# Kernel optimization log

Measured on AMD Instinct MI355X. Metric: run time of the kernel, lower is better.

Reference implementation:

```python
import math
import jax, jax.numpy as jnp
import numpy as np

D_MODEL = 1024
N_HEADS = 16
HEAD_DIM = D_MODEL // N_HEADS  # 64
QDIM = HEAD_DIM // 4           # 16
SPIKE_SLOPE = 5.0
B, S = 2, 2048


def _qweight(r, i, j, k):
    # Hamilton-product weight matrix, identical to QLinear.forward's torch.cat construction.
    return jnp.concatenate([
        jnp.concatenate([r, -i, -j, -k], 1),
        jnp.concatenate([i, r, -k, j], 1),
        jnp.concatenate([j, k, r, -i], 1),
        jnp.concatenate([k, -j, i, r], 1),
    ], 0)


def setup_inputs() -> dict:
    key = jax.random.key(0)
    ks = jax.random.split(key, 20)
    Qo = Qi = D_MODEL // 4  # 256
    p = lambda k, shape, s=0.02: (jax.random.normal(k, shape, dtype=jnp.float32) * s)
    inp = {
        'query': jax.random.normal(ks[0], (B, S, D_MODEL), dtype=jnp.float32),
        'key_in': jax.random.normal(ks[1], (B, S, D_MODEL), dtype=jnp.float32),
        'value': jax.random.normal(ks[2], (B, S, D_MODEL), dtype=jnp.float32),
        'mask': jnp.ones((B, S), dtype=jnp.int32),
        'density_feat': jax.random.normal(ks[3], (B, S, 3), dtype=jnp.float32),
        # q_proj QLinear params
        'wq_r': p(ks[4], (Qo, Qi)), 'wq_i': p(ks[5], (Qo, Qi)),
        'wq_j': p(ks[6], (Qo, Qi)), 'wq_k': p(ks[7], (Qo, Qi)),
        'bq': jnp.zeros((D_MODEL,), jnp.float32),
        # k_proj QLinear params
        'wk_r': p(ks[8], (Qo, Qi)), 'wk_i': p(ks[9], (Qo, Qi)),
        'wk_j': p(ks[10], (Qo, Qi)), 'wk_k': p(ks[11], (Qo, Qi)),
        'bk': jnp.zeros((D_MODEL,), jnp.float32),
        # v_proj / out_proj dense params
        'wv': p(ks[12], (D_MODEL, D_MODEL)), 'bv': jnp.zeros((D_MODEL,), jnp.float32),
        'wo': p(ks[13], (D_MODEL, D_MODEL)), 'bo': jnp.zeros((D_MODEL,), jnp.float32),
        # learned spike threshold (init -1.0 as in torch)
        'threshold': jnp.asarray(-1.0, dtype=jnp.float32),
        # density_mod MLP (use nonzero values so the gate shift is exercised)
        'dm1_w': p(ks[14], (16, 3), 0.5), 'dm1_b': p(ks[15], (16,), 0.1),
        'dm2_w': p(ks[16], (1, 16), 0.5), 'dm2_b': p(ks[17], (1,), 0.1),
    }
    return inp


def reference(query, key_in, value, mask, density_feat,
              wq_r, wq_i, wq_j, wq_k, bq,
              wk_r, wk_i, wk_j, wk_k, bk,
              wv, bv, wo, bo, threshold,
              dm1_w, dm1_b, dm2_w, dm2_b):
    H, hd, Qd = N_HEADS, HEAD_DIM, QDIM
    Bq, Sq, D = query.shape

    Wq = _qweight(wq_r, wq_i, wq_j, wq_k)
    Wk = _qweight(wk_r, wk_i, wk_j, wk_k)
    q = query @ Wq.T + bq
    k = key_in @ Wk.T + bk
    v = value @ wv.T + bv

    # head-major split, matching torch.cat(x.split(hd, -1), dim=0)
    qh = q.reshape(Bq, Sq, H, hd).transpose(2, 0, 1, 3)  # (H,B,S,hd)
    kh = k.reshape(Bq, Sq, H, hd).transpose(2, 0, 1, 3)
    vh = v.reshape(Bq, Sq, H, hd).transpose(2, 0, 1, 3)

    # sum of 4 quaternion-component dot products == full dot product over hd
    scores = jnp.einsum('hbmd,hbnd->hbmn', qh, kh) / math.sqrt(Qd)
    scores = jnp.clip(scores, -6.0, 6.0)

    base_threshold = jax.nn.softplus(threshold)
    h1 = jax.nn.gelu(density_feat @ dm1_w.T + dm1_b, approximate=False)
    d_shift = (h1 @ dm2_w.T + dm2_b)[..., 0]  # (B,N)
    thr = base_threshold + d_shift[None, :, None, :] * 0.1  # (1,B,1,N)

    spike_gate = jax.nn.sigmoid(SPIKE_SLOPE * (scores - thr))
    mod = scores * (1.0 + spike_gate * 2.0)

    m2 = (mask[:, :, None] * mask[:, None, :])[None]  # (1,B,N,N)
    mod = jnp.where(m2 == 0, -10000.0, mod)

    weights = jax.nn.softmax(jnp.clip(mod, -30.0, 30.0), axis=-1)
    # dropout: eval mode (identity)
    out_h = jnp.einsum('hbmn,hbnd->hbmd', weights, vh)
    out = out_h.transpose(1, 2, 0, 3).reshape(Bq, Sq, D)
    return out @ wo.T + bo
```

## Files before the change

### kernel.cpp

```cpp
#include <hip/hip_runtime.h>
#include <stdint.h>
#include <math.h>

#define BB 2
#define SS 2048
#define DM 1024
#define NH 16
#define HD 64
#define MTOT (BB*SS)

typedef __bf16 bf16x8 __attribute__((ext_vector_type(8)));
typedef float  f32x4  __attribute__((ext_vector_type(4)));
typedef uint32_t u32x4 __attribute__((ext_vector_type(4)));

__device__ __forceinline__ unsigned short f2bf(float f) {
  __bf16 h = (__bf16)f;
  return __builtin_bit_cast(unsigned short, h);
}

__device__ __forceinline__ bf16x8 ldsv8(const unsigned short* p) {
  return __builtin_bit_cast(bf16x8, *(const u32x4*)p);
}

__device__ __forceinline__ void gl16(const void* g, void* l) {
  __builtin_amdgcn_global_load_lds(
      (const __attribute__((address_space(1))) uint32_t*)g,
      (__attribute__((address_space(3))) uint32_t*)l, 16, 0, 0);
}

#define MFMA16(a,b,c) __builtin_amdgcn_mfma_f32_16x16x32_bf16((a),(b),(c),0,0,0)

#define C_NEG5L2E  (-7.213475204444817f)
#define C_L2E      (1.4426950408889634f)
#define C_18L2E    (25.968510736001341f)

__global__ __launch_bounds__(256) void cvt_bf16(
    const float* __restrict__ a, const float* __restrict__ b, const float* __restrict__ c,
    unsigned short* __restrict__ ao, unsigned short* __restrict__ bo, unsigned short* __restrict__ co)
{
  const int i8 = (blockIdx.x * 256 + threadIdx.x) * 8;
  {
    const float4 f0 = *(const float4*)(a + i8);
    const float4 f1 = *(const float4*)(a + i8 + 4);
    union { unsigned short us[8]; u32x4 v; } t;
    t.us[0]=f2bf(f0.x); t.us[1]=f2bf(f0.y); t.us[2]=f2bf(f0.z); t.us[3]=f2bf(f0.w);
    t.us[4]=f2bf(f1.x); t.us[5]=f2bf(f1.y); t.us[6]=f2bf(f1.z); t.us[7]=f2bf(f1.w);
    *(u32x4*)(ao + i8) = t.v;
  }
  {
    const float4 f0 = *(const float4*)(b + i8);
    const float4 f1 = *(const float4*)(b + i8 + 4);
    union { unsigned short us[8]; u32x4 v; } t;
    t.us[0]=f2bf(f0.x); t.us[1]=f2bf(f0.y); t.us[2]=f2bf(f0.z); t.us[3]=f2bf(f0.w);
    t.us[4]=f2bf(f1.x); t.us[5]=f2bf(f1.y); t.us[6]=f2bf(f1.z); t.us[7]=f2bf(f1.w);
    *(u32x4*)(bo + i8) = t.v;
  }
  {
    const float4 f0 = *(const float4*)(c + i8);
    const float4 f1 = *(const float4*)(c + i8 + 4);
    union { unsigned short us[8]; u32x4 v; } t;
    t.us[0]=f2bf(f0.x); t.us[1]=f2bf(f0.y); t.us[2]=f2bf(f0.z); t.us[3]=f2bf(f0.w);
    t.us[4]=f2bf(f1.x); t.us[5]=f2bf(f1.y); t.us[6]=f2bf(f1.z); t.us[7]=f2bf(f1.w);
    *(u32x4*)(co + i8) = t.v;
  }
}

__global__ __launch_bounds__(256) void prep_w(
    const float* __restrict__ wqr, const float* __restrict__ wqi,
    const float* __restrict__ wqj, const float* __restrict__ wqk,
    const float* __restrict__ wkr, const float* __restrict__ wki,
    const float* __restrict__ wkj, const float* __restrict__ wkk,
    const float* __restrict__ wv,  const float* __restrict__ wo,
    unsigned short* __restrict__ Wq, unsigned short* __restrict__ Wk,
    unsigned short* __restrict__ Wv, unsigned short* __restrict__ Wo)
{
  const int idx = blockIdx.x * 256 + threadIdx.x;
  const int o = idx >> 10, i = idx & 1023;
  const int br = o >> 8, bc = i >> 8;
  const int ro = o & 255, ci = i & 255;
  const int comp[4][4] = {{0,1,2,3},{1,0,3,2},{2,3,0,1},{3,2,1,0}};
  const float sgn[4][4] = {{1.f,-1.f,-1.f,-1.f},{1.f,1.f,-1.f,1.f},{1.f,1.f,1.f,-1.f},{1.f,-1.f,1.f,1.f}};
  const float* pq[4] = {wqr, wqi, wqj, wqk};
  const float* pk[4] = {wkr, wki, wkj, wkk};
  const int c_ = comp[br][bc];
  const float s_ = sgn[br][bc];
  const int pidx = ro * 256 + ci;
  Wq[idx] = f2bf(s_ * pq[c_][pidx]);
  Wk[idx] = f2bf(s_ * pk[c_][pidx]);
  Wv[idx] = f2bf(wv[idx]);
  Wo[idx] = f2bf(wo[idx]);
}

__global__ __launch_bounds__(256) void prep_thr(
    const float* __restrict__ density, const float* __restrict__ dm1w,
    const float* __restrict__ dm1b, const float* __restrict__ dm2w,
    const float* __restrict__ dm2b, const float* __restrict__ thr_s,
    const int* __restrict__ mask, float2* __restrict__ out)
{
  const int i = blockIdx.x * 256 + threadIdx.x;
  if (i >= BB * SS) return;
  const float x0 = density[i*3+0], x1 = density[i*3+1], x2 = density[i*3+2];
  const float base = log1pf(expf(thr_s[0]));
  float acc = dm2b[0];
  #pragma unroll
  for (int j = 0; j < 16; ++j) {
    const float hj = dm1w[j*3+0]*x0 + dm1w[j*3+1]*x1 + dm1w[j*3+2]*x2 + dm1b[j];
    const float ge = 0.5f * hj * (1.0f + erff(hj * 0.70710678118654752f));
    acc += dm2w[j] * ge;
  }
  const float thr = base + 0.1f * acc;
  out[i] = make_float2(thr * (-C_NEG5L2E),
                       mask[i] ? 1e30f : -30.0f);
}

struct GemmArgs {
  const unsigned short* A[3];
  const unsigned short* W[3];
  const float* bias[3];
  void* out[3];
  float scale[3];
  int omode[3];
};

template<int DB>
__global__ __launch_bounds__(256) void gemm_bt(GemmArgs args)
{
  __shared__ __align__(16) unsigned short lA[DB + 1][128*64];
  __shared__ __align__(16) unsigned short lB[DB + 1][128*64];
  const int z = blockIdx.y;
  const int tid = threadIdx.x;
  const int wid = tid >> 6, lane = tid & 63;
  const int l15 = lane & 15, l4 = lane >> 4;
  const int bm = blockIdx.x & 31, bn = blockIdx.x >> 5;
  const int row0 = bm * 128, col0 = bn * 128;
  const int wm = (wid >> 1) * 64, wn = (wid & 1) * 64;

  const unsigned short* gA[4];
  const unsigned short* gB[4];
  #pragma unroll
  for (int i = 0; i < 4; ++i) {
    const int c = (wid * 4 + i) * 64 + lane;
    const int r = c >> 3, jx = c & 7, j = jx ^ (r & 7);
    gA[i] = args.A[z] + (row0 + r) * 1024 + j * 8;
    gB[i] = args.W[z] + (col0 + r) * 1024 + j * 8;
  }

  f32x4 acc[4][4];
  #pragma unroll
  for (int i = 0; i < 4; ++i)
    #pragma unroll
    for (int j = 0; j < 4; ++j) acc[i][j] = (f32x4){0.f,0.f,0.f,0.f};

  #pragma unroll
  for (int i = 0; i < 4; ++i) {
    gl16(gA[i], &lA[0][(wid * 4 + i) * 512]);
    gl16(gB[i], &lB[0][(wid * 4 + i) * 512]);
  }
  if (DB) __syncthreads();

  for (int kt = 0; kt < 16; ++kt) {
    const int cb = DB ? (kt & 1) : 0;
    if (DB) {
      if (kt < 15) {
        const int nb = cb ^ 1, k0 = (kt + 1) * 64;
        #pragma unroll
        for (int i = 0; i < 4; ++i) {
          gl16(gA[i] + k0, &lA[nb][(wid * 4 + i) * 512]);
          gl16(gB[i] + k0, &lB[nb][(wid * 4 + i) * 512]);
        }
      }
    } else {
      if (kt > 0) {
        const int k0 = kt * 64;
        #pragma unroll
        for (int i = 0; i < 4; ++i) {
          gl16(gA[i] + k0, &lA[0][(wid * 4 + i) * 512]);
          gl16(gB[i] + k0, &lB[0][(wid * 4 + i) * 512]);
        }
      }
      __syncthreads();
    }
    #pragma unroll
    for (int kk = 0; kk < 2; ++kk) {
      const int kl = kk * 32 + l4 * 8;
      bf16x8 af[4], bfb[4];
      #pragma unroll
      for (int mi = 0; mi < 4; ++mi) {
        const int r = wm + mi * 16 + l15;
        af[mi] = ldsv8(&lA[cb][r * 64 + (kl ^ ((r & 7) << 3))]);
      }
      #pragma unroll
      for (int nj = 0; nj < 4; ++nj) {
        const int r = wn + nj * 16 + l15;
        bfb[nj] = ldsv8(&lB[cb][r * 64 + (kl ^ ((r & 7) << 3))]);
      }
      #pragma unroll
      for (int mi = 0; mi < 4; ++mi)
        #pragma unroll
        for (int nj = 0; nj < 4; ++nj)
          acc[mi][nj] = MFMA16(af[mi], bfb[nj], acc[mi][nj]);
    }
    __syncthreads();
  }

  const int om = args.omode[z];
  const float sc = args.scale[z];
  void* Cptr = args.out[z];
  #pragma unroll
  for (int nj = 0; nj < 4; ++nj) {
    const int c = col0 + wn + nj * 16 + l15;
    const float bv_ = args.bias[z][c];
    #pragma unroll
    for (int mi = 0; mi < 4; ++mi) {
      const int rb = row0 + wm + mi * 16 + l4 * 4;
      #pragma unroll
      for (int e = 0; e < 4; ++e) {
        const float val = (acc[mi][nj][e] + bv_) * sc;
        const int r = rb + e;
        if (om == 0) {
          ((unsigned short*)Cptr)[r * 1024 + c] = f2bf(val);
        } else if (om == 2) {
          ((float*)Cptr)[r * 1024 + c] = val;
        } else {
          const int h = c >> 6, d = c & 63, b = r >> 11, s = r & 2047;
          ((unsigned short*)Cptr)[((h * BB + b) * HD + d) * SS + s] = f2bf(val);
        }
      }
    }
  }
}

__global__ __launch_bounds__(512) void attn_kernel(
    const unsigned short* __restrict__ qg, const unsigned short* __restrict__ kg,
    const unsigned short* __restrict__ vT, const float2* __restrict__ klim,
    const int* __restrict__ mask, unsigned short* __restrict__ outg)
{
  __shared__ __align__(16) unsigned short smem[20480];
  unsigned short* lK = smem;
  unsigned short* lV = smem + 8192;
  unsigned short* lP = smem + 16384;

  const int tid = threadIdx.x;
  const int wid = tid >> 6, lane = tid & 63;
  const int l15 = lane & 15, l4 = lane >> 4;
  const int rg = wid >> 1, par = wid & 1;
  const int hb = blockIdx.x & 31, qb = blockIdx.x >> 5;
  const int h = hb >> 1, b = hb & 1;
  const int qr0 = qb * 64 + rg * 16;

  const int kcr = tid >> 3, kcj = (tid & 7) * 8;
  const int vcd = tid >> 3, vck = (tid & 7) * 8;
  const int kdst = (kcr >> 5) * 2048 + (kcr & 31) * 64 + (kcj ^ ((((kcr & 31) >> 1) & 7) << 3));
  const int vdst = (vck >> 5) * 2048 + vcd * 32 + ((vck & 31) ^ ((vcd & 3) << 3));

  const unsigned short* kbase = kg + (b * SS) * DM + h * HD;
  const unsigned short* vbase = vT + ((h * BB + b) * HD) * SS;
  const float2* klimb = klim + b * SS;

  bf16x8 aq[2];
  {
    const unsigned short* qs = qg + (b * SS + qr0 + l15) * DM + h * HD + l4 * 8;
    aq[0] = __builtin_bit_cast(bf16x8, *(const u32x4*)qs);
    aq[1] = __builtin_bit_cast(bf16x8, *(const u32x4*)(qs + 32));
  }
  float limq[4];
  #pragma unroll
  for (int e = 0; e < 4; ++e)
    limq[e] = mask[b * SS + qr0 + l4 * 4 + e] ? 1e30f : -30.0f;

  float lrun[4] = {0.f, 0.f, 0.f, 0.f};
  f32x4 o[4];
  #pragma unroll
  for (int d = 0; d < 4; ++d) o[d] = (f32x4){0.f,0.f,0.f,0.f};

  unsigned short* lPw = lP + wid * 512;

  u32x4 kr = *(const u32x4*)(kbase + kcr * DM + kcj);
  u32x4 vr = *(const u32x4*)(vbase + vcd * SS + vck);
  *(u32x4*)&lK[kdst] = kr;
  *(u32x4*)&lV[vdst] = vr;
  __syncthreads();

  for (int pr = 0; pr < 32; ++pr) {
    const int cur = pr & 1;
    const unsigned short* lKt = lK + cur * 4096 + par * 2048;
    const unsigned short* lVt = lV + cur * 4096 + par * 2048;
    const int n0 = pr * 64 + par * 32;

    if (pr < 31) {
      const int nn = (pr + 1) * 64;
      kr = *(const u32x4*)(kbase + (nn + kcr) * DM + kcj);
      vr = *(const u32x4*)(vbase + vcd * SS + nn + vck);
    }

    const float4 klA = *(const float4*)(klimb + n0 + 2 * l15);

    f32x4 sv[2];
    __builtin_amdgcn_s_setprio(1);
    #pragma unroll
    for (int cf = 0; cf < 2; ++cf) {
      f32x4 a = (f32x4){0.f,0.f,0.f,0.f};
      const int r = 2 * l15 + cf;
      #pragma unroll
      for (int kk = 0; kk < 2; ++kk)
        a = MFMA16(aq[kk], ldsv8(&lKt[r * 64 + ((kk * 32 + l4 * 8) ^ ((l15 & 7) << 3))]), a);
      sv[cf] = a;
    }
    __builtin_amdgcn_s_setprio(0);

    float pvv[2][4];
    #pragma unroll
    for (int cf = 0; cf < 2; ++cf) {
      const float kth = cf ? klA.z : klA.x;
      const float klm = cf ? klA.w : klA.y;
      #pragma unroll
      for (int e = 0; e < 4; ++e) {
        float s = fminf(fmaxf(sv[cf][e], -6.f), 6.f);
        const float t = __builtin_amdgcn_exp2f(fmaf(s, C_NEG5L2E, kth));
        const float g = __builtin_amdgcn_rcpf(1.f + t);
        float md = fmaf(s + s, g, s);
        md = fminf(md, fminf(klm, limq[e]));
        const float p = __builtin_amdgcn_exp2f(fmaf(md, C_L2E, -C_18L2E));
        pvv[cf][e] = p;
        lrun[e] += p;
      }
    }

    #pragma unroll
    for (int e = 0; e < 4; ++e) {
      const int rr = l4 * 4 + e;
      union { unsigned short us[2]; unsigned int u; } pk2;
      pk2.us[0] = f2bf(pvv[0][e]);
      pk2.us[1] = f2bf(pvv[1][e]);
      *(unsigned int*)&lPw[rr * 32 + ((2 * l15) ^ ((rr & 3) << 3))] = pk2.u;
    }
    asm volatile("s_waitcnt lgkmcnt(0)" ::: "memory");
    __builtin_amdgcn_sched_barrier(0);

    const bf16x8 pa = ldsv8(&lPw[l15 * 32 + ((l4 * 8) ^ ((l15 & 3) << 3))]);

    __builtin_amdgcn_s_setprio(1);
    #pragma unroll
    for (int df = 0; df < 4; ++df) {
      const int d = df * 16 + l15;
      o[df] = MFMA16(pa, ldsv8(&lVt[d * 32 + ((l4 * 8) ^ ((d & 3) << 3))]), o[df]);
    }
    __builtin_amdgcn_s_setprio(0);

    if (pr < 31) {
      const int nxt = cur ^ 1;
      *(u32x4*)&lK[nxt * 4096 + kdst] = kr;
      *(u32x4*)&lV[nxt * 4096 + vdst] = vr;
    }
    __syncthreads();
  }

  __syncthreads();
  float* xch = (float*)smem;
  float* slot = xch + rg * 1280;
  if (par) {
    #pragma unroll
    for (int df = 0; df < 4; ++df)
      *(f32x4*)&slot[(df * 64 + lane) * 4] = o[df];
    f32x4 lr;
    lr[0] = lrun[0]; lr[1] = lrun[1]; lr[2] = lrun[2]; lr[3] = lrun[3];
    *(f32x4*)&slot[1024 + lane * 4] = lr;
  }
  __syncthreads();
  if (!par) {
    #pragma unroll
    for (int df = 0; df < 4; ++df) {
      const f32x4 t = *(const f32x4*)&slot[(df * 64 + lane) * 4];
      o[df][0] += t[0]; o[df][1] += t[1]; o[df][2] += t[2]; o[df][3] += t[3];
    }
    const f32x4 lr = *(const f32x4*)&slot[1024 + lane * 4];
    #pragma unroll
    for (int e = 0; e < 4; ++e) {
      float ls = lrun[e] + lr[e];
      ls += __shfl_xor(ls, 1);
      ls += __shfl_xor(ls, 2);
      ls += __shfl_xor(ls, 4);
      ls += __shfl_xor(ls, 8);
      const float rl = __builtin_amdgcn_rcpf(ls);
      const int r = qr0 + l4 * 4 + e;
      #pragma unroll
      for (int df = 0; df < 4; ++df) {
        outg[(b * SS + r) * DM + h * HD + df * 16 + l15] = f2bf(o[df][e] * rl);
      }
    }
  }
}

extern "C" void kernel_launch(void* const* d_in, const int* in_sizes, int n_in,
                              void* d_out, int out_size, void* d_ws, size_t ws_size,
                              hipStream_t stream)
{
  const float* query   = (const float*)d_in[0];
  const float* key_in  = (const float*)d_in[1];
  const float* value   = (const float*)d_in[2];
  const int*   mask    = (const int*)d_in[3];
  const float* density = (const float*)d_in[4];
  const float* wq_r = (const float*)d_in[5];
  const float* wq_i = (const float*)d_in[6];
  const float* wq_j = (const float*)d_in[7];
  const float* wq_k = (const float*)d_in[8];
  const float* bq   = (const float*)d_in[9];
  const float* wk_r = (const float*)d_in[10];
  const float* wk_i = (const float*)d_in[11];
  const float* wk_j = (const float*)d_in[12];
  const float* wk_k = (const float*)d_in[13];
  const float* bk   = (const float*)d_in[14];
  const float* wv   = (const float*)d_in[15];
  const float* bv   = (const float*)d_in[16];
  const float* wo   = (const float*)d_in[17];
  const float* bo   = (const float*)d_in[18];
  const float* thrs = (const float*)d_in[19];
  const float* dm1w = (const float*)d_in[20];
  const float* dm1b = (const float*)d_in[21];
  const float* dm2w = (const float*)d_in[22];
  const float* dm2b = (const float*)d_in[23];

  char* ws = (char*)d_ws;
  unsigned short* Wq  = (unsigned short*)(ws + ((size_t)0 << 20));
  unsigned short* Wk  = (unsigned short*)(ws + ((size_t)2 << 20));
  unsigned short* Wv  = (unsigned short*)(ws + ((size_t)4 << 20));
  unsigned short* Wo  = (unsigned short*)(ws + ((size_t)6 << 20));
  unsigned short* qbf = (unsigned short*)(ws + ((size_t)8 << 20));
  unsigned short* kbf = (unsigned short*)(ws + ((size_t)16 << 20));
  unsigned short* vT  = (unsigned short*)(ws + ((size_t)24 << 20));
  unsigned short* att = (unsigned short*)(ws + ((size_t)32 << 20));
  float2* klim        = (float2*)(ws + ((size_t)40 << 20));

  unsigned short* qcv = (unsigned short*)d_out;
  unsigned short* kcv = (unsigned short*)d_out + (size_t)MTOT * DM;
  unsigned short* vcv = att;

  cvt_bf16<<<2048, 256, 0, stream>>>(query, key_in, value, qcv, kcv, vcv);
  prep_w<<<4096, 256, 0, stream>>>(wq_r, wq_i, wq_j, wq_k,
                                   wk_r, wk_i, wk_j, wk_k,
                                   wv, wo, Wq, Wk, Wv, Wo);
  prep_thr<<<16, 256, 0, stream>>>(density, dm1w, dm1b, dm2w, dm2b, thrs, mask, klim);

  GemmArgs qkv;
  qkv.A[0] = qcv; qkv.W[0] = Wq; qkv.bias[0] = bq; qkv.out[0] = qbf; qkv.scale[0] = 0.25f; qkv.omode[0] = 0;
  qkv.A[1] = kcv; qkv.W[1] = Wk; qkv.bias[1] = bk; qkv.out[1] = kbf; qkv.scale[1] = 1.0f;  qkv.omode[1] = 0;
  qkv.A[2] = vcv; qkv.W[2] = Wv; qkv.bias[2] = bv; qkv.out[2] = vT;  qkv.scale[2] = 1.0f;  qkv.omode[2] = 1;
  gemm_bt<0><<<dim3(256, 3), 256, 0, stream>>>(qkv);

  attn_kernel<<<1024, 512, 0, stream>>>(qbf, kbf, vT, klim, mask, att);

  GemmArgs og;
  og.A[0] = att; og.W[0] = Wo; og.bias[0] = bo; og.out[0] = d_out; og.scale[0] = 1.0f; og.omode[0] = 2;
  og.A[1] = att; og.W[1] = Wo; og.bias[1] = bo; og.out[1] = d_out; og.scale[1] = 1.0f; og.omode[1] = 2;
  og.A[2] = att; og.W[2] = Wo; og.bias[2] = bo; og.out[2] = d_out; og.scale[2] = 1.0f; og.omode[2] = 2;
  gemm_bt<1><<<dim3(256, 1), 256, 0, stream>>>(og);
}
```

Measured before the change: 188.3 us.

## Rework attention to 32x32 MFMA with register P exchange and mask-free fast path

The attention kernel switches from 16x16x32 to 32x32x16 MFMA tiles, with each block covering 128 query rows. The P matrix is now passed between lanes with cross-lane shuffles instead of a round trip through LDS. Key thresholds and mask limits are staged in LDS alongside K/V. A per-64-key bitmap built in prep_thr lets tiles with no masked keys skip the key-mask min. The aim is fewer LDS round trips and instructions per tile, in exchange for half as many blocks and more register pressure.

After: 233.5 us. 24.0% more time.

```diff
diff --git a/kernel.cpp b/kernel.cpp
--- a/kernel.cpp
+++ b/kernel.cpp
@@ -11,6 +11,7 @@
 
 typedef __bf16 bf16x8 __attribute__((ext_vector_type(8)));
 typedef float  f32x4  __attribute__((ext_vector_type(4)));
+typedef float  f32x16 __attribute__((ext_vector_type(16)));
 typedef uint32_t u32x4 __attribute__((ext_vector_type(4)));
 
 __device__ __forceinline__ unsigned short f2bf(float f) {
@@ -29,6 +30,7 @@
 }
 
 #define MFMA16(a,b,c) __builtin_amdgcn_mfma_f32_16x16x32_bf16((a),(b),(c),0,0,0)
+#define MFMA32(a,b,c) __builtin_amdgcn_mfma_f32_32x32x16_bf16((a),(b),(c),0,0,0)
 
 #define C_NEG5L2E  (-7.213475204444817f)
 #define C_L2E      (1.4426950408889634f)
@@ -95,7 +97,8 @@
     const float* __restrict__ density, const float* __restrict__ dm1w,
     const float* __restrict__ dm1b, const float* __restrict__ dm2w,
     const float* __restrict__ dm2b, const float* __restrict__ thr_s,
-    const int* __restrict__ mask, float2* __restrict__ out)
+    const int* __restrict__ mask, float* __restrict__ kth,
+    float* __restrict__ klm, unsigned int* __restrict__ fbits)
 {
   const int i = blockIdx.x * 256 + threadIdx.x;
   if (i >= BB * SS) return;
@@ -109,8 +112,12 @@
     acc += dm2w[j] * ge;
   }
   const float thr = base + 0.1f * acc;
-  out[i] = make_float2(thr * (-C_NEG5L2E),
-                       mask[i] ? 1e30f : -30.0f);
+  const int mk = mask[i];
+  kth[i] = thr * (-C_NEG5L2E);
+  klm[i] = mk ? 1e30f : -30.0f;
+  const unsigned long long any = __ballot(mk == 0);
+  if ((threadIdx.x & 63) == 0 && any)
+    atomicOr(&fbits[i >> 11], 1u << ((i >> 6) & 31));
 }
 
 struct GemmArgs {
@@ -230,163 +237,199 @@
   }
 }
 
-__global__ __launch_bounds__(512) void attn_kernel(
+__global__ __launch_bounds__(512, 4) void attn_kernel(
     const unsigned short* __restrict__ qg, const unsigned short* __restrict__ kg,
-    const unsigned short* __restrict__ vT, const float2* __restrict__ klim,
-    const int* __restrict__ mask, unsigned short* __restrict__ outg)
+    const unsigned short* __restrict__ vT, const float* __restrict__ kth_g,
+    const float* __restrict__ klm_g, const unsigned int* __restrict__ fbits,
+    unsigned short* __restrict__ outg)
 {
-  __shared__ __align__(16) unsigned short smem[20480];
-  unsigned short* lK = smem;
-  unsigned short* lV = smem + 8192;
-  unsigned short* lP = smem + 16384;
-
+  __shared__ __align__(16) unsigned char smem[36864];
   const int tid = threadIdx.x;
-  const int wid = tid >> 6, lane = tid & 63;
-  const int l15 = lane & 15, l4 = lane >> 4;
+  const int lane = tid & 63, wid = tid >> 6;
+  const int l31 = lane & 31, l5 = lane >> 5;
   const int rg = wid >> 1, par = wid & 1;
-  const int hb = blockIdx.x & 31, qb = blockIdx.x >> 5;
+  const int hb = blockIdx.x & 31, qc = blockIdx.x >> 5;
   const int h = hb >> 1, b = hb & 1;
-  const int qr0 = qb * 64 + rg * 16;
-
-  const int kcr = tid >> 3, kcj = (tid & 7) * 8;
-  const int vcd = tid >> 3, vck = (tid & 7) * 8;
-  const int kdst = (kcr >> 5) * 2048 + (kcr & 31) * 64 + (kcj ^ ((((kcr & 31) >> 1) & 7) << 3));
-  const int vdst = (vck >> 5) * 2048 + vcd * 32 + ((vck & 31) ^ ((vcd & 3) << 3));
-
-  const unsigned short* kbase = kg + (b * SS) * DM + h * HD;
-  const unsigned short* vbase = vT + ((h * BB + b) * HD) * SS;
-  const float2* klimb = klim + b * SS;
-
-  bf16x8 aq[2];
+  const int qr0 = qc * 128 + rg * 32;
+
+  const unsigned short* kbase = kg + (size_t)(b * SS) * DM + h * HD;
+  const unsigned short* vbase = vT + (size_t)((h * BB + b) * HD) * SS;
+  const float* kthb = kth_g + b * SS;
+  const float* klmb = klm_g + b * SS;
+  const unsigned int fb = fbits[b];
+
+  const int sk = tid >> 3, sj = tid & 7;
+  const int kp = sk >> 5, kkl = sk & 31;
+  const int kdst = kp*4096 + (kkl>>1)*256 + (((((kkl&1)<<3)|sj)) ^ ((kkl>>1)&15))*16;
+  const int vp = sj >> 2, vjj = sj & 3;
+  const int vdst = 8192 + vp*4096 + (sk>>2)*256 + (((((sk&3)<<2)|vjj)) ^ ((sk>>2)&15))*16;
+  const unsigned short* kgsrc = kbase + sk * DM + sj * 8;
+  const unsigned short* vgsrc = vbase + (size_t)sk * SS + sj * 8;
+
+  bf16x8 bq[4];
   {
-    const unsigned short* qs = qg + (b * SS + qr0 + l15) * DM + h * HD + l4 * 8;
-    aq[0] = __builtin_bit_cast(bf16x8, *(const u32x4*)qs);
-    aq[1] = __builtin_bit_cast(bf16x8, *(const u32x4*)(qs + 32));
-  }
-  float limq[4];
-  #pragma unroll
-  for (int e = 0; e < 4; ++e)
-    limq[e] = mask[b * SS + qr0 + l4 * 4 + e] ? 1e30f : -30.0f;
-
-  float lrun[4] = {0.f, 0.f, 0.f, 0.f};
-  f32x4 o[4];
-  #pragma unroll
-  for (int d = 0; d < 4; ++d) o[d] = (f32x4){0.f,0.f,0.f,0.f};
-
-  unsigned short* lPw = lP + wid * 512;
-
-  u32x4 kr = *(const u32x4*)(kbase + kcr * DM + kcj);
-  u32x4 vr = *(const u32x4*)(vbase + vcd * SS + vck);
-  *(u32x4*)&lK[kdst] = kr;
-  *(u32x4*)&lV[vdst] = vr;
+    const unsigned short* qs = qg + (size_t)(b * SS + qr0 + l31) * DM + h * HD + l5 * 8;
+    #pragma unroll
+    for (int ks = 0; ks < 4; ++ks)
+      bq[ks] = __builtin_bit_cast(bf16x8, *(const u32x4*)(qs + ks * 16));
+  }
+  const float limq = klmb[qr0 + l31];
+
+  f32x16 O0 = {}, O1 = {};
+  float lsum = 0.f;
+
+  u32x4 kr = *(const u32x4*)kgsrc;
+  u32x4 vr = *(const u32x4*)vgsrc;
+  f32x4 tk, tl;
+  if (tid < 16)      tk = *(const f32x4*)(kthb + tid * 4);
+  else if (tid < 32) tl = *(const f32x4*)(klmb + (tid - 16) * 4);
+  *(u32x4*)(smem + kdst) = kr;
+  *(u32x4*)(smem + vdst) = vr;
+  if (tid < 16)      *(f32x4*)(smem + 16384 + tid * 16) = tk;
+  else if (tid < 32) *(f32x4*)(smem + 16640 + (tid - 16) * 16) = tl;
   __syncthreads();
 
   for (int pr = 0; pr < 32; ++pr) {
-    const int cur = pr & 1;
-    const unsigned short* lKt = lK + cur * 4096 + par * 2048;
-    const unsigned short* lVt = lV + cur * 4096 + par * 2048;
-    const int n0 = pr * 64 + par * 32;
+    unsigned char* cb = smem + (pr & 1) * 16896;
+    const int n0 = pr * 64;
 
     if (pr < 31) {
-      const int nn = (pr + 1) * 64;
-      kr = *(const u32x4*)(kbase + (nn + kcr) * DM + kcj);
-      vr = *(const u32x4*)(vbase + vcd * SS + nn + vck);
-    }
-
-    const float4 klA = *(const float4*)(klimb + n0 + 2 * l15);
-
-    f32x4 sv[2];
-    __builtin_amdgcn_s_setprio(1);
-    #pragma unroll
-    for (int cf = 0; cf < 2; ++cf) {
-      f32x4 a = (f32x4){0.f,0.f,0.f,0.f};
-      const int r = 2 * l15 + cf;
-      #pragma unroll
-      for (int kk = 0; kk < 2; ++kk)
-        a = MFMA16(aq[kk], ldsv8(&lKt[r * 64 + ((kk * 32 + l4 * 8) ^ ((l15 & 7) << 3))]), a);
-      sv[cf] = a;
-    }
-    __builtin_amdgcn_s_setprio(0);
-
-    float pvv[2][4];
-    #pragma unroll
-    for (int cf = 0; cf < 2; ++cf) {
-      const float kth = cf ? klA.z : klA.x;
-      const float klm = cf ? klA.w : klA.y;
-      #pragma unroll
-      for (int e = 0; e < 4; ++e) {
-        float s = fminf(fmaxf(sv[cf][e], -6.f), 6.f);
-        const float t = __builtin_amdgcn_exp2f(fmaf(s, C_NEG5L2E, kth));
+      kr = *(const u32x4*)(kgsrc + (size_t)(n0 + 64) * DM);
+      vr = *(const u32x4*)(vgsrc + n0 + 64);
+      if (tid < 16)      tk = *(const f32x4*)(kthb + n0 + 64 + tid * 4);
+      else if (tid < 32) tl = *(const f32x4*)(klmb + n0 + 64 + (tid - 16) * 4);
+    }
+
+    f32x4 kth4[4];
+    #pragma unroll
+    for (int g2 = 0; g2 < 4; ++g2)
+      kth4[g2] = *(const f32x4*)(cb + 16384 + par*128 + g2*32 + l5*16);
+
+    f32x16 S = {};
+    {
+      const unsigned char* Kb = cb + par * 4096;
+      const int krow = l31 >> 1;
+      __builtin_amdgcn_s_setprio(1);
+      #pragma unroll
+      for (int ks = 0; ks < 4; ++ks) {
+        const int slot = ((((l31 & 1) << 3) | (ks*2 + l5)) ^ (krow & 15));
+        bf16x8 ka = __builtin_bit_cast(bf16x8, *(const u32x4*)(Kb + krow*256 + slot*16));
+        S = MFMA32(ka, bq[ks], S);
+      }
+      __builtin_amdgcn_s_setprio(0);
+    }
+
+    float p[16];
+    if (!((fb >> pr) & 1)) {
+      #pragma unroll
+      for (int r = 0; r < 16; ++r) {
+        float s = fminf(fmaxf(S[r], -6.f), 6.f);
+        const float t = __builtin_amdgcn_exp2f(fmaf(s, C_NEG5L2E, kth4[r>>2][r&3]));
         const float g = __builtin_amdgcn_rcpf(1.f + t);
         float md = fmaf(s + s, g, s);
-        md = fminf(md, fminf(klm, limq[e]));
-        const float p = __builtin_amdgcn_exp2f(fmaf(md, C_L2E, -C_18L2E));
-        pvv[cf][e] = p;
-        lrun[e] += p;
-      }
-    }
-
-    #pragma unroll
-    for (int e = 0; e < 4; ++e) {
-      const int rr = l4 * 4 + e;
-      union { unsigned short us[2]; unsigned int u; } pk2;
-      pk2.us[0] = f2bf(pvv[0][e]);
-      pk2.us[1] = f2bf(pvv[1][e]);
-      *(unsigned int*)&lPw[rr * 32 + ((2 * l15) ^ ((rr & 3) << 3))] = pk2.u;
-    }
-    asm volatile("s_waitcnt lgkmcnt(0)" ::: "memory");
-    __builtin_amdgcn_sched_barrier(0);
-
-    const bf16x8 pa = ldsv8(&lPw[l15 * 32 + ((l4 * 8) ^ ((l15 & 3) << 3))]);
-
-    __builtin_amdgcn_s_setprio(1);
-    #pragma unroll
-    for (int df = 0; df < 4; ++df) {
-      const int d = df * 16 + l15;
-      o[df] = MFMA16(pa, ldsv8(&lVt[d * 32 + ((l4 * 8) ^ ((d & 3) << 3))]), o[df]);
-    }
-    __builtin_amdgcn_s_setprio(0);
+        md = fminf(md, limq);
+        const float pv = __builtin_amdgcn_exp2f(fmaf(md, C_L2E, -C_18L2E));
+        p[r] = pv;
+        lsum += pv;
+      }
+    } else {
+      f32x4 klm4[4];
+      #pragma unroll
+      for (int g2 = 0; g2 < 4; ++g2)
+        klm4[g2] = *(const f32x4*)(cb + 16640 + par*128 + g2*32 + l5*16);
+      #pragma unroll
+      for (int r = 0; r < 16; ++r) {
+        float s = fminf(fmaxf(S[r], -6.f), 6.f);
+        const float t = __builtin_amdgcn_exp2f(fmaf(s, C_NEG5L2E, kth4[r>>2][r&3]));
+        const float g = __builtin_amdgcn_rcpf(1.f + t);
+        float md = fmaf(s + s, g, s);
+        md = fminf(md, fminf(klm4[r>>2][r&3], limq));
+        const float pv = __builtin_amdgcn_exp2f(fmaf(md, C_L2E, -C_18L2E));
+        p[r] = pv;
+        lsum += pv;
+      }
+    }
+
+    unsigned int c[8], cp[8];
+    #pragma unroll
+    for (int i = 0; i < 8; ++i) {
+      union { unsigned short us[2]; unsigned int u; } t2;
+      t2.us[0] = f2bf(p[2*i]); t2.us[1] = f2bf(p[2*i+1]);
+      c[i] = t2.u;
+    }
+    #pragma unroll
+    for (int i = 0; i < 8; ++i) cp[i] = (unsigned int)__shfl_xor((int)c[i], 32);
+    bf16x8 pa0, pa1;
+    {
+      union { unsigned int u[4]; bf16x8 v; } fa;
+      fa.u[0] = l5 ? cp[2] : c[0];
+      fa.u[1] = l5 ? cp[3] : c[1];
+      fa.u[2] = l5 ? c[2]  : cp[0];
+      fa.u[3] = l5 ? c[3]  : cp[1];
+      pa0 = fa.v;
+      fa.u[0] = l5 ? cp[6] : c[4];
+      fa.u[1] = l5 ? cp[7] : c[5];
+      fa.u[2] = l5 ? c[6]  : cp[4];
+      fa.u[3] = l5 ? c[7]  : cp[5];
+      pa1 = fa.v;
+    }
+
+    {
+      const unsigned char* Vb = cb + 8192 + par * 4096;
+      __builtin_amdgcn_s_setprio(1);
+      #pragma unroll
+      for (int dt = 0; dt < 2; ++dt) {
+        const int vrow = dt*8 + (l31 >> 2);
+        #pragma unroll
+        for (int ks2 = 0; ks2 < 2; ++ks2) {
+          const int slot = ((((l31 & 3) << 2) | (ks2*2 + l5)) ^ (vrow & 15));
+          bf16x8 bv = __builtin_bit_cast(bf16x8, *(const u32x4*)(Vb + vrow*256 + slot*16));
+          if (dt == 0) O0 = MFMA32(ks2 ? pa1 : pa0, bv, O0);
+          else         O1 = MFMA32(ks2 ? pa1 : pa0, bv, O1);
+        }
+      }
+      __builtin_amdgcn_s_setprio(0);
+    }
 
     if (pr < 31) {
-      const int nxt = cur ^ 1;
-      *(u32x4*)&lK[nxt * 4096 + kdst] = kr;
-      *(u32x4*)&lV[nxt * 4096 + vdst] = vr;
+      unsigned char* nb = smem + ((pr + 1) & 1) * 16896;
+      *(u32x4*)(nb + kdst) = kr;
+      *(u32x4*)(nb + vdst) = vr;
+      if (tid < 16)      *(f32x4*)(nb + 16384 + tid * 16) = tk;
+      else if (tid < 32) *(f32x4*)(nb + 16640 + (tid - 16) * 16) = tl;
     }
     __syncthreads();
   }
 
+  float* xf = (float*)smem;
+  xf[(rg*2 + par)*64 + lane] = lsum;
   __syncthreads();
-  float* xch = (float*)smem;
-  float* slot = xch + rg * 1280;
+  float* dinv = (float*)(smem + 2048);
+  if (par == 0 && lane < 32) {
+    const float* ls0 = xf + rg * 128;
+    const float den = ls0[lane] + ls0[32 + lane] + ls0[64 + lane] + ls0[96 + lane];
+    dinv[rg*32 + lane] = __builtin_amdgcn_rcpf(den);
+  }
+  __syncthreads();
+  float* od = (float*)(smem + 4096) + rg * 2048;
   if (par) {
     #pragma unroll
-    for (int df = 0; df < 4; ++df)
-      *(f32x4*)&slot[(df * 64 + lane) * 4] = o[df];
-    f32x4 lr;
-    lr[0] = lrun[0]; lr[1] = lrun[1]; lr[2] = lrun[2]; lr[3] = lrun[3];
-    *(f32x4*)&slot[1024 + lane * 4] = lr;
+    for (int r = 0; r < 16; ++r) {
+      od[r*64 + lane]        = O0[r];
+      od[(16 + r)*64 + lane] = O1[r];
+    }
   }
   __syncthreads();
   if (!par) {
-    #pragma unroll
-    for (int df = 0; df < 4; ++df) {
-      const f32x4 t = *(const f32x4*)&slot[(df * 64 + lane) * 4];
-      o[df][0] += t[0]; o[df][1] += t[1]; o[df][2] += t[2]; o[df][3] += t[3];
-    }
-    const f32x4 lr = *(const f32x4*)&slot[1024 + lane * 4];
-    #pragma unroll
-    for (int e = 0; e < 4; ++e) {
-      float ls = lrun[e] + lr[e];
-      ls += __shfl_xor(ls, 1);
-      ls += __shfl_xor(ls, 2);
-      ls += __shfl_xor(ls, 4);
-      ls += __shfl_xor(ls, 8);
-      const float rl = __builtin_amdgcn_rcpf(ls);
-      const int r = qr0 + l4 * 4 + e;
-      #pragma unroll
-      for (int df = 0; df < 4; ++df) {
-        outg[(b * SS + r) * DM + h * HD + df * 16 + l15] = f2bf(o[df][e] * rl);
-      }
+    unsigned short* ob = outg + (size_t)(b * SS + qr0) * DM + h * HD;
+    #pragma unroll
+    for (int r = 0; r < 16; ++r) {
+      const int row = (r & 3) + 8*(r >> 2) + 4*l5;
+      const float di = dinv[rg*32 + row];
+      const float v0 = O0[r] + od[r*64 + lane];
+      const float v1 = O1[r] + od[(16 + r)*64 + lane];
+      ob[(size_t)row * DM + l31]      = f2bf(v0 * di);
+      ob[(size_t)row * DM + 32 + l31] = f2bf(v1 * di);
     }
   }
 }
@@ -429,17 +472,21 @@
   unsigned short* kbf = (unsigned short*)(ws + ((size_t)16 << 20));
   unsigned short* vT  = (unsigned short*)(ws + ((size_t)24 << 20));
   unsigned short* att = (unsigned short*)(ws + ((size_t)32 << 20));
-  float2* klim        = (float2*)(ws + ((size_t)40 << 20));
+  float* kth_g        = (float*)(ws + ((size_t)40 << 20));
+  float* klm_g        = (float*)(ws + ((size_t)40 << 20) + 16384);
+  unsigned int* fbits = (unsigned int*)(ws + ((size_t)40 << 20) + 32768);
 
   unsigned short* qcv = (unsigned short*)d_out;
   unsigned short* kcv = (unsigned short*)d_out + (size_t)MTOT * DM;
   unsigned short* vcv = att;
 
+  hipMemsetAsync(fbits, 0, 2 * sizeof(unsigned int), stream);
   cvt_bf16<<<2048, 256, 0, stream>>>(query, key_in, value, qcv, kcv, vcv);
   prep_w<<<4096, 256, 0, stream>>>(wq_r, wq_i, wq_j, wq_k,
                                    wk_r, wk_i, wk_j, wk_k,
                                    wv, wo, Wq, Wk, Wv, Wo);
-  prep_thr<<<16, 256, 0, stream>>>(density, dm1w, dm1b, dm2w, dm2b, thrs, mask, klim);
+  prep_thr<<<16, 256, 0, stream>>>(density, dm1w, dm1b, dm2w, dm2b, thrs, mask,
+                                   kth_g, klm_g, fbits);
 
   GemmArgs qkv;
   qkv.A[0] = qcv; qkv.W[0] = Wq; qkv.bias[0] = bq; qkv.out[0] = qbf; qkv.scale[0] = 0.25f; qkv.omode[0] = 0;
@@ -447,7 +494,7 @@
   qkv.A[2] = vcv; qkv.W[2] = Wv; qkv.bias[2] = bv; qkv.out[2] = vT;  qkv.scale[2] = 1.0f;  qkv.omode[2] = 1;
   gemm_bt<0><<<dim3(256, 3), 256, 0, stream>>>(qkv);
 
-  attn_kernel<<<1024, 512, 0, stream>>>(qbf, kbf, vT, klim, mask, att);
+  attn_kernel<<<512, 512, 0, stream>>>(qbf, kbf, vT, kth_g, klm_g, fbits, att);
 
   GemmArgs og;
   og.A[0] = att; og.W[0] = Wo; og.bias[0] = bo; og.out[0] = d_out; og.scale[0] = 1.0f; og.omode[0] = 2;
```
